# Kernel tuning notes

Measured on AMD Instinct MI355X. Metric: run time of the kernel, lower is better.

The kernel has to match this reference:

```python
import jax, jax.numpy as jnp
import numpy as np


def setup_inputs() -> dict:
    key = jax.random.key(0)
    k1, k2 = jax.random.split(key)
    B, IN, OUT = 4096, 4096, 4096
    x = jax.random.normal(k1, (B, IN), dtype=jnp.float32)
    W = jax.random.normal(k2, (OUT, IN), dtype=jnp.float32) * (1.0 / np.sqrt(IN))
    return {"x": x, "W": W, "k": 128}


def reference(x, W, k):
    # temp = (x[:, None, :] * W).sum(axis=1)  ==  x * W.sum(axis=0)  -> [B, in]
    # (the original materializes the O(B*out*in) intermediate; math is identical)
    temp = jax.lax.stop_gradient(x) * jnp.sum(W, axis=0)  # x_vals is detached in torch
    _, idx_top = jax.lax.top_k(jnp.abs(temp), k)          # [B, k] indices into `in` dim
    B = x.shape[0]
    z = jnp.ones_like(x).at[jnp.arange(B)[:, None], idx_top].set(0.0)
    out = jnp.matmul(x * z, W.T)                          # [B, out]
    return out
```

## Files before the change

### kernel.cpp

```cpp
#include <hip/hip_runtime.h>
#include <hip/hip_bf16.h>
#include <stdint.h>

#define B_DIM   4096
#define IN_DIM  4096
#define OUT_DIM 4096
#define K_SEL   128

typedef unsigned short u16;
typedef __bf16 bf16x8 __attribute__((ext_vector_type(8)));
typedef float  f32x4  __attribute__((ext_vector_type(4)));

static __device__ __forceinline__ u16 f2bf(float f) {
    uint32_t u = __builtin_bit_cast(uint32_t, f);
    uint32_t r = (u + 0x7fffu + ((u >> 16) & 1u)) >> 16;
    return (u16)r;
}

__global__ __launch_bounds__(256) void colsum_conv(const float* __restrict__ W,
                                                   double* __restrict__ part,
                                                   u16* __restrict__ Wb) {
    int cb = blockIdx.x & 3;
    int rb = blockIdx.x >> 2;
    int c4 = cb * 256 + threadIdx.x;
    int row0 = rb * 8;
    double s0 = 0.0, s1 = 0.0, s2 = 0.0, s3 = 0.0;
    for (int r = 0; r < 8; ++r) {
        const float4 v = ((const float4*)(W + (size_t)(row0 + r) * IN_DIM))[c4];
        s0 += (double)v.x; s1 += (double)v.y; s2 += (double)v.z; s3 += (double)v.w;
        ushort4 o;
        o.x = f2bf(v.x); o.y = f2bf(v.y); o.z = f2bf(v.z); o.w = f2bf(v.w);
        ((ushort4*)(Wb + (size_t)(row0 + r) * IN_DIM))[c4] = o;
    }
    double4 d; d.x = s0; d.y = s1; d.z = s2; d.w = s3;
    ((double4*)(part + (size_t)rb * IN_DIM))[c4] = d;
}

__global__ __launch_bounds__(256) void colsum_final(const double* __restrict__ part,
                                                    float* __restrict__ cs) {
    __shared__ double red[256];
    const int t = threadIdx.x;
    const int c = blockIdx.x * 16 + (t & 15);
    const int g = t >> 4;
    double s = 0.0;
    for (int r = 0; r < 32; ++r) s += part[(size_t)(g * 32 + r) * IN_DIM + c];
    red[t] = s;
    __syncthreads();
    for (int off = 128; off >= 16; off >>= 1) {
        if (t < off) red[t] += red[t + off];
        __syncthreads();
    }
    if (t < 16) cs[blockIdx.x * 16 + t] = (float)red[t];
}

__global__ __launch_bounds__(256) void topk_mask(const float* __restrict__ x,
                                                 const float* __restrict__ cs,
                                                 u16* __restrict__ xz) {
    __shared__ uint32_t hist[256];
    __shared__ uint32_t suf[256];
    __shared__ uint32_t s_scan[256];
    __shared__ uint32_t s_prefix, s_krem;

    const int b = blockIdx.x, t = threadIdx.x;
    const float4* xrow = (const float4*)(x + (size_t)b * IN_DIM);
    const float4* csv  = (const float4*)cs;

    float    xr[16];
    uint32_t ul[16];
#pragma unroll
    for (int q = 0; q < 4; ++q) {
        float4 xv = xrow[t * 4 + q];
        float4 cv = csv[t * 4 + q];
        xr[q*4+0] = xv.x; xr[q*4+1] = xv.y; xr[q*4+2] = xv.z; xr[q*4+3] = xv.w;
        ul[q*4+0] = __builtin_bit_cast(uint32_t, xv.x * cv.x) & 0x7fffffffu;
        ul[q*4+1] = __builtin_bit_cast(uint32_t, xv.y * cv.y) & 0x7fffffffu;
        ul[q*4+2] = __builtin_bit_cast(uint32_t, xv.z * cv.z) & 0x7fffffffu;
        ul[q*4+3] = __builtin_bit_cast(uint32_t, xv.w * cv.w) & 0x7fffffffu;
    }
    if (t == 0) { s_prefix = 0u; s_krem = K_SEL; }
    __syncthreads();

#pragma unroll
    for (int p = 3; p >= 0; --p) {
        const int sh = p * 8;
        const uint32_t hi_mask = (p == 3) ? 0u : (0xFFFFFFFFu << (sh + 8));
        const uint32_t prefix = s_prefix;
        const uint32_t krem   = s_krem;
        hist[t] = 0u;
        __syncthreads();
#pragma unroll
        for (int j = 0; j < 16; ++j) {
            uint32_t u = ul[j];
            if ((u & hi_mask) == (prefix & hi_mask))
                atomicAdd(&hist[(u >> sh) & 255u], 1u);
        }
        __syncthreads();
        uint32_t mine = hist[t];
        suf[t] = mine;
        __syncthreads();
#pragma unroll
        for (int off = 1; off < 256; off <<= 1) {
            uint32_t other = (t + off < 256) ? suf[t + off] : 0u;
            __syncthreads();
            mine += other;
            suf[t] = mine;
            __syncthreads();
        }
        uint32_t mysuf   = suf[t];
        uint32_t nextsuf = (t < 255) ? suf[t + 1] : 0u;
        if (mysuf >= krem && (t == 255 || nextsuf < krem)) {
            s_prefix = prefix | ((uint32_t)t << sh);
            s_krem   = krem - nextsuf;
        }
        __syncthreads();
    }
    const uint32_t T       = s_prefix;
    const uint32_t need_eq = s_krem;

    int cnt = 0;
#pragma unroll
    for (int j = 0; j < 16; ++j) cnt += (ul[j] == T) ? 1 : 0;
    s_scan[t] = (uint32_t)cnt;
    __syncthreads();
    uint32_t inc = (uint32_t)cnt;
#pragma unroll
    for (int off = 1; off < 256; off <<= 1) {
        uint32_t other = (t >= off) ? s_scan[t - off] : 0u;
        __syncthreads();
        inc += other;
        s_scan[t] = inc;
        __syncthreads();
    }
    const int base = (int)(inc - (uint32_t)cnt);

    union { u16 us[16]; uint4 v[2]; } ob;
    int eqseen = 0;
#pragma unroll
    for (int j = 0; j < 16; ++j) {
        uint32_t u = ul[j];
        bool drop = (u > T);
        if (u == T) {
            if (base + eqseen < (int)need_eq) drop = true;
            ++eqseen;
        }
        ob.us[j] = drop ? (u16)0 : f2bf(xr[j]);
    }
    uint4* dst = (uint4*)(xz + (size_t)b * IN_DIM + t * 16);
    dst[0] = ob.v[0];
    dst[1] = ob.v[1];
}

#define NT 64

__global__ __launch_bounds__(512, 2) void gemm_pl(const u16* __restrict__ A,
                                                  const u16* __restrict__ Bm,
                                                  float* __restrict__ C) {
    __shared__ u16 lds_[65536];

    const int bid = blockIdx.x;
    const int swz = (bid & 7) * 32 + (bid >> 3);
    const int m0 = (swz >> 4) * 256, n0 = (swz & 15) * 256;

    const int t = threadIdx.x;
    const int l = t & 63;
    const int lr = l & 15, lk = l >> 4;
    const int w = t >> 6;
    const int wm = w >> 2, wn = w & 3;

    const int cswz = ((t & 7) ^ ((t >> 3) & 7)) * 8;
    const int c0   = (lk ^ (lr & 7)) * 8;
    const int c1   = c0 ^ 32;

    f32x4 acc[8][4];
#pragma unroll
    for (int i = 0; i < 8; ++i)
#pragma unroll
        for (int j = 0; j < 4; ++j) acc[i][j] = f32x4{0.f, 0.f, 0.f, 0.f};

#define GLOAD(g, off_bytes)                                                     \
    __builtin_amdgcn_global_load_lds(                                           \
        (const __attribute__((address_space(1))) void*)(g),                     \
        (__attribute__((address_space(3))) void*)(((char*)lds_) + (off_bytes)), \
        16, 0, 0)

    auto stA = [&](int kb, int r, int kt) {
#pragma unroll
        for (int g = 0; g < 2; ++g)
            GLOAD(A + (size_t)(m0 + g * 128 + r * 64 + (t >> 3)) * IN_DIM + kt + cswz,
                  kb * 65536 + r * 16384 + g * 8192 + t * 16);
    };
    auto stB = [&](int kb, int r, int kt) {
#pragma unroll
        for (int g = 0; g < 2; ++g)
            GLOAD(Bm + (size_t)(n0 + r * 128 + g * 64 + (t >> 3)) * IN_DIM + kt + cswz,
                  kb * 65536 + 32768 + r * 16384 + g * 8192 + t * 16);
    };

    auto rdA = [&](bf16x8 (&dst)[4], int bufo, int qm, int c) {
#pragma unroll
        for (int mi = 0; mi < 4; ++mi)
            dst[mi] = *(const bf16x8*)&lds_[bufo + qm * 8192 + wm * 4096 + lr * 64 + mi * 1024 + c];
    };
    auto rdB = [&](bf16x8 (&dst)[4], int bufo, int c) {
#pragma unroll
        for (int ni = 0; ni < 4; ++ni)
            dst[ni] = *(const bf16x8*)&lds_[bufo + 16384 + (wn >> 1) * 8192 + (wn & 1) * 4096 + lr * 64 + ni * 1024 + c];
    };
    auto mm = [&](int base, bf16x8 (&Aa)[4], bf16x8 (&Bb)[4]) {
        __builtin_amdgcn_s_setprio(1);
#pragma unroll
        for (int mi = 0; mi < 4; ++mi)
#pragma unroll
            for (int ni = 0; ni < 4; ++ni)
                acc[base + mi][ni] = __builtin_amdgcn_mfma_f32_16x16x32_bf16(
                    Aa[mi], Bb[ni], acc[base + mi][ni], 0, 0, 0);
        __builtin_amdgcn_s_setprio(0);
        __builtin_amdgcn_sched_barrier(0);
    };

    bf16x8 a0k0[4], a0k1[4], a1k0[4], a1k1[4], bk0[4], bk1[4];

    stA(0, 0, 0); stA(0, 1, 0); stB(0, 0, 0); stB(0, 1, 0);
    stA(1, 0, 64); stB(1, 0, 64); stB(1, 1, 64);
    asm volatile("s_waitcnt vmcnt(6)" ::: "memory");
    __builtin_amdgcn_s_barrier();
    asm volatile("" ::: "memory");
    rdA(a0k0, 0, 0, c0);
    rdB(bk0, 0, c0);

    for (int k = 0; k < NT; ++k) {
        const int bufo = (k & 1) * 32768;
        const int bufno = bufo ^ 32768;
        const int kbC = k & 1, kbN = kbC ^ 1;
        const int kt1 = (k + 1) * 64, kt2 = (k + 2) * 64;

        rdA(a0k1, bufo, 0, c1);
        rdB(bk1, bufo, c1);
        if (k < NT - 1) stA(kbN, 1, kt1);
        mm(0, a0k0, bk0);
        asm volatile("" ::: "memory");
        __builtin_amdgcn_s_barrier();
        asm volatile("" ::: "memory");

        rdA(a1k0, bufo, 1, c0);
        rdA(a1k1, bufo, 1, c1);
        mm(0, a0k1, bk1);
        asm volatile("" ::: "memory");
        __builtin_amdgcn_s_barrier();
        asm volatile("" ::: "memory");

        if (k < NT - 2) { stA(kbC, 0, kt2); stB(kbC, 0, kt2); }
        mm(4, a1k0, bk0);
        if (k < NT - 2) {
            asm volatile("s_waitcnt vmcnt(4)" ::: "memory");
        } else {
            asm volatile("s_waitcnt vmcnt(0)" ::: "memory");
        }
        __builtin_amdgcn_s_barrier();
        asm volatile("" ::: "memory");

        if (k < NT - 1) {
            rdA(a0k0, bufno, 0, c0);
            rdB(bk0, bufno, c0);
        }
        if (k < NT - 2) stB(kbC, 1, kt2);
        mm(4, a1k1, bk1);
        asm volatile("" ::: "memory");
        __builtin_amdgcn_s_barrier();
        asm volatile("" ::: "memory");
    }
#undef GLOAD

#pragma unroll
    for (int gmi = 0; gmi < 8; ++gmi)
#pragma unroll
        for (int ni = 0; ni < 4; ++ni)
#pragma unroll
            for (int r = 0; r < 4; ++r) {
                int row = m0 + wm * 128 + (gmi >> 2) * 64 + (gmi & 3) * 16 + lk * 4 + r;
                int col = n0 + wn * 64 + ni * 16 + lr;
                C[(size_t)row * OUT_DIM + col] = acc[gmi][ni][r];
            }
}

extern "C" void kernel_launch(void* const* d_in, const int* in_sizes, int n_in,
                              void* d_out, int out_size, void* d_ws, size_t ws_size,
                              hipStream_t stream) {
    const float* x = (const float*)d_in[0];
    const float* W = (const float*)d_in[1];
    float* out = (float*)d_out;

    char* ws = (char*)d_ws;
    u16*    Wb   = (u16*)ws;
    u16*    xz   = (u16*)(ws + (size_t)32 * 1024 * 1024);
    float*  cs   = (float*)(ws + (size_t)64 * 1024 * 1024);
    double* part = (double*)d_out;

    colsum_conv<<<2048, 256, 0, stream>>>(W, part, Wb);
    colsum_final<<<256, 256, 0, stream>>>(part, cs);
    topk_mask<<<4096, 256, 0, stream>>>(x, cs, xz);
    gemm_pl<<<256, 512, 0, stream>>>(xz, Wb, out);
}
```

Measured before the change: 188.9 us.

## Restructure GEMM main loop into four quadrant phases with full-K fragment reads

The bf16 GEMM main loop is reorganized so each iteration runs four MFMA phases over (M-half, N-half) quadrants. Each quadrant reads both K-halves of its A/B fragments, rather than splitting work along K. Global-to-LDS loads for the next stages are interleaved across the phases, with explicit lgkmcnt waits and more barriers. The aim is better reuse of the loaded fragments and steadier overlap of loads with MFMA work. The cost is more barriers per iteration and a changed LDS read pattern that could add stalls.

New measurement: 187.7 us. No clear change (-0.6%).

```diff
diff --git a/kernel.cpp b/kernel.cpp
--- a/kernel.cpp
+++ b/kernel.cpp
@@ -152,7 +152,7 @@
 
 #define NT 64
 
-__global__ __launch_bounds__(512, 2) void gemm_pl(const u16* __restrict__ A,
+__global__ __launch_bounds__(512, 2) void gemm_m2(const u16* __restrict__ A,
                                                   const u16* __restrict__ Bm,
                                                   float* __restrict__ C) {
     __shared__ u16 lds_[65536];
@@ -183,89 +183,108 @@
         (__attribute__((address_space(3))) void*)(((char*)lds_) + (off_bytes)), \
         16, 0, 0)
 
-    auto stA = [&](int kb, int r, int kt) {
+    auto stA = [&](int kb, int h, int kt) {
 #pragma unroll
         for (int g = 0; g < 2; ++g)
-            GLOAD(A + (size_t)(m0 + g * 128 + r * 64 + (t >> 3)) * IN_DIM + kt + cswz,
-                  kb * 65536 + r * 16384 + g * 8192 + t * 16);
-    };
-    auto stB = [&](int kb, int r, int kt) {
+            GLOAD(A + (size_t)(m0 + h * 128 + g * 64 + (t >> 3)) * IN_DIM + kt + cswz,
+                  kb * 65536 + h * 16384 + g * 8192 + t * 16);
+    };
+    auto stB = [&](int kb, int h, int kt) {
 #pragma unroll
         for (int g = 0; g < 2; ++g)
-            GLOAD(Bm + (size_t)(n0 + r * 128 + g * 64 + (t >> 3)) * IN_DIM + kt + cswz,
-                  kb * 65536 + 32768 + r * 16384 + g * 8192 + t * 16);
-    };
-
-    auto rdA = [&](bf16x8 (&dst)[4], int bufo, int qm, int c) {
+            GLOAD(Bm + (size_t)(n0 + h * 128 + g * 64 + (t >> 3)) * IN_DIM + kt + cswz,
+                  kb * 65536 + 32768 + h * 16384 + g * 8192 + t * 16);
+    };
+
+    auto rdA = [&](bf16x8 (&dst)[4][2], int bufo, int qm) {
+#pragma unroll
+        for (int mi = 0; mi < 4; ++mi) {
+            int ro = bufo + wm * 8192 + (qm * 64 + mi * 16 + lr) * 64;
+            dst[mi][0] = *(const bf16x8*)&lds_[ro + c0];
+            dst[mi][1] = *(const bf16x8*)&lds_[ro + c1];
+        }
+    };
+    auto rdB = [&](bf16x8 (&dst)[2][2], int bufo, int qn) {
+#pragma unroll
+        for (int n2 = 0; n2 < 2; ++n2) {
+            int ro = bufo + 16384 + (wn >> 1) * 8192 + ((wn & 1) * 64 + qn * 32 + n2 * 16 + lr) * 64;
+            dst[n2][0] = *(const bf16x8*)&lds_[ro + c0];
+            dst[n2][1] = *(const bf16x8*)&lds_[ro + c1];
+        }
+    };
+    auto mm = [&](int mb, int nb, bf16x8 (&Aa)[4][2], bf16x8 (&Bb)[2][2]) {
+        __builtin_amdgcn_s_setprio(1);
 #pragma unroll
         for (int mi = 0; mi < 4; ++mi)
-            dst[mi] = *(const bf16x8*)&lds_[bufo + qm * 8192 + wm * 4096 + lr * 64 + mi * 1024 + c];
-    };
-    auto rdB = [&](bf16x8 (&dst)[4], int bufo, int c) {
-#pragma unroll
-        for (int ni = 0; ni < 4; ++ni)
-            dst[ni] = *(const bf16x8*)&lds_[bufo + 16384 + (wn >> 1) * 8192 + (wn & 1) * 4096 + lr * 64 + ni * 1024 + c];
-    };
-    auto mm = [&](int base, bf16x8 (&Aa)[4], bf16x8 (&Bb)[4]) {
-        __builtin_amdgcn_s_setprio(1);
-#pragma unroll
-        for (int mi = 0; mi < 4; ++mi)
-#pragma unroll
-            for (int ni = 0; ni < 4; ++ni)
-                acc[base + mi][ni] = __builtin_amdgcn_mfma_f32_16x16x32_bf16(
-                    Aa[mi], Bb[ni], acc[base + mi][ni], 0, 0, 0);
+#pragma unroll
+            for (int n2 = 0; n2 < 2; ++n2) {
+                acc[mb + mi][nb + n2] = __builtin_amdgcn_mfma_f32_16x16x32_bf16(
+                    Aa[mi][0], Bb[n2][0], acc[mb + mi][nb + n2], 0, 0, 0);
+                acc[mb + mi][nb + n2] = __builtin_amdgcn_mfma_f32_16x16x32_bf16(
+                    Aa[mi][1], Bb[n2][1], acc[mb + mi][nb + n2], 0, 0, 0);
+            }
         __builtin_amdgcn_s_setprio(0);
         __builtin_amdgcn_sched_barrier(0);
     };
 
-    bf16x8 a0k0[4], a0k1[4], a1k0[4], a1k1[4], bk0[4], bk1[4];
-
-    stA(0, 0, 0); stA(0, 1, 0); stB(0, 0, 0); stB(0, 1, 0);
-    stA(1, 0, 64); stB(1, 0, 64); stB(1, 1, 64);
+    bf16x8 A0[4][2], A1[4][2], B0[2][2], B1[2][2];
+
+    stA(0, 0, 0);  stA(0, 1, 0);  stB(0, 0, 0);  stB(0, 1, 0);
+    stA(1, 0, 64); stA(1, 1, 64); stB(1, 0, 64);
     asm volatile("s_waitcnt vmcnt(6)" ::: "memory");
     __builtin_amdgcn_s_barrier();
     asm volatile("" ::: "memory");
-    rdA(a0k0, 0, 0, c0);
-    rdB(bk0, 0, c0);
 
     for (int k = 0; k < NT; ++k) {
         const int bufo = (k & 1) * 32768;
-        const int bufno = bufo ^ 32768;
-        const int kbC = k & 1, kbN = kbC ^ 1;
+        const int cur = k & 1, nxt = cur ^ 1;
         const int kt1 = (k + 1) * 64, kt2 = (k + 2) * 64;
 
-        rdA(a0k1, bufo, 0, c1);
-        rdB(bk1, bufo, c1);
-        if (k < NT - 1) stA(kbN, 1, kt1);
-        mm(0, a0k0, bk0);
-        asm volatile("" ::: "memory");
-        __builtin_amdgcn_s_barrier();
-        asm volatile("" ::: "memory");
-
-        rdA(a1k0, bufo, 1, c0);
-        rdA(a1k1, bufo, 1, c1);
-        mm(0, a0k1, bk1);
-        asm volatile("" ::: "memory");
-        __builtin_amdgcn_s_barrier();
-        asm volatile("" ::: "memory");
-
-        if (k < NT - 2) { stA(kbC, 0, kt2); stB(kbC, 0, kt2); }
-        mm(4, a1k0, bk0);
+        rdA(A0, bufo, 0);
+        rdB(B0, bufo, 0);
+        if (k < NT - 1) stB(nxt, 1, kt1);
+        asm volatile("s_waitcnt lgkmcnt(8)" ::: "memory");
+        __builtin_amdgcn_s_barrier();
+        asm volatile("s_waitcnt lgkmcnt(0)" ::: "memory");
+        __builtin_amdgcn_sched_barrier(0);
+        mm(0, 0, A0, B0);
+        asm volatile("" ::: "memory");
+        __builtin_amdgcn_s_barrier();
+        asm volatile("" ::: "memory");
+
+        rdA(A1, bufo, 1);
+        if (k < NT - 2) stA(cur, 0, kt2);
+        asm volatile("" ::: "memory");
+        __builtin_amdgcn_s_barrier();
+        asm volatile("s_waitcnt lgkmcnt(0)" ::: "memory");
+        __builtin_amdgcn_sched_barrier(0);
+        mm(4, 0, A1, B0);
+        asm volatile("" ::: "memory");
+        __builtin_amdgcn_s_barrier();
+        asm volatile("" ::: "memory");
+
+        rdB(B1, bufo, 1);
+        if (k < NT - 2) stA(cur, 1, kt2);
+        asm volatile("" ::: "memory");
+        __builtin_amdgcn_s_barrier();
+        asm volatile("s_waitcnt lgkmcnt(0)" ::: "memory");
+        __builtin_amdgcn_sched_barrier(0);
+        mm(4, 2, A1, B1);
+        asm volatile("" ::: "memory");
+        __builtin_amdgcn_s_barrier();
+        asm volatile("" ::: "memory");
+
+        if (k < NT - 2) stB(cur, 0, kt2);
+        asm volatile("" ::: "memory");
+        __builtin_amdgcn_s_barrier();
+        asm volatile("" ::: "memory");
+        __builtin_amdgcn_sched_barrier(0);
+        mm(0, 2, A0, B1);
         if (k < NT - 2) {
-            asm volatile("s_waitcnt vmcnt(4)" ::: "memory");
-        } else {
+            asm volatile("s_waitcnt vmcnt(6)" ::: "memory");
+        } else if (k == NT - 2) {
             asm volatile("s_waitcnt vmcnt(0)" ::: "memory");
         }
-        __builtin_amdgcn_s_barrier();
-        asm volatile("" ::: "memory");
-
-        if (k < NT - 1) {
-            rdA(a0k0, bufno, 0, c0);
-            rdB(bk0, bufno, c0);
-        }
-        if (k < NT - 2) stB(kbC, 1, kt2);
-        mm(4, a1k1, bk1);
-        asm volatile("" ::: "memory");
         __builtin_amdgcn_s_barrier();
         asm volatile("" ::: "memory");
     }
@@ -299,5 +318,5 @@
     colsum_conv<<<2048, 256, 0, stream>>>(W, part, Wb);
     colsum_final<<<256, 256, 0, stream>>>(part, cs);
     topk_mask<<<4096, 256, 0, stream>>>(x, cs, xz);
-    gemm_pl<<<256, 512, 0, stream>>>(xz, Wb, out);
-}
+    gemm_m2<<<256, 512, 0, stream>>>(xz, Wb, out);
+}
```
